# Kernel optimization log

Measured on AMD Instinct MI355X. Metric: run time of the kernel, lower is better.

## Reference

```python
import jax, jax.numpy as jnp
import numpy as np

N_HEADS = 16
D_EMBED = 1024
D_CROSS = 768
D_HEAD = D_EMBED // N_HEADS
B, S = 4, 2048


def setup_inputs() -> dict:
    key = jax.random.key(0)
    ks = jax.random.split(key, 10)
    sq = lambda k, shp, fan: jax.random.normal(k, shp, jnp.float32) / np.sqrt(fan)
    return {
        "x": jax.random.normal(ks[0], (B, S, D_EMBED), jnp.float32),
        "y": jax.random.normal(ks[1], (B, S, D_CROSS), jnp.float32),
        "Wq": sq(ks[2], (D_EMBED, D_EMBED), D_EMBED),
        "bq": jnp.zeros((D_EMBED,), jnp.float32),
        "Wk": sq(ks[3], (D_CROSS, D_EMBED), D_CROSS),
        "bk": jnp.zeros((D_EMBED,), jnp.float32),
        "Wv": sq(ks[4], (D_CROSS, D_EMBED), D_CROSS),
        "bv": jnp.zeros((D_EMBED,), jnp.float32),
        "Wo": sq(ks[5], (D_EMBED, D_EMBED), D_EMBED),
        "bo": jnp.zeros((D_EMBED,), jnp.float32),
    }


def reference(x, y, Wq, bq, Wk, bk, Wv, bv, Wo, bo):
    b, s, _ = y.shape
    q = x @ Wq + bq  # [b, s, d_embed]
    k = y @ Wk + bk
    v = y @ Wv + bv
    # [b, h, s, d_head]
    q = q.reshape(b, s, N_HEADS, D_HEAD).transpose(0, 2, 1, 3)
    k = k.reshape(b, s, N_HEADS, D_HEAD).transpose(0, 2, 1, 3)
    v = v.reshape(b, s, N_HEADS, D_HEAD).transpose(0, 2, 1, 3)
    scale = 1.0 / np.sqrt(D_HEAD).astype(np.float32)
    scores = jnp.einsum("bhqd,bhkd->bhqk", q, k) * scale
    weights = jax.nn.softmax(scores, axis=-1)
    out = jnp.einsum("bhqk,bhkd->bhqd", weights, v)
    out = out.transpose(0, 2, 1, 3).reshape(x.shape)
    return out @ Wo + bo
```

## Files before the change

### kernel.cpp

```cpp
#include <hip/hip_runtime.h>

#define NHEADS 16
#define DEMBED 1024
#define DCROSS 768
#define DHEAD  64
#define BATCH  4
#define SLEN   2048
#define MROWS  (BATCH * SLEN)

using bf16   = __bf16;
using bf16x8 = __attribute__((ext_vector_type(8))) __bf16;
using bf16x4 = __attribute__((ext_vector_type(4))) __bf16;
using bf16x2 = __attribute__((ext_vector_type(2))) __bf16;
using f32x4  = __attribute__((ext_vector_type(4))) float;
using f32x16 = __attribute__((ext_vector_type(16))) float;

__device__ __forceinline__ f32x4 mfma_bf16(bf16x8 a, bf16x8 b, f32x4 c) {
    return __builtin_amdgcn_mfma_f32_16x16x32_bf16(a, b, c, 0, 0, 0);
}
__device__ __forceinline__ f32x16 mfma32(bf16x8 a, bf16x8 b, f32x16 c) {
    return __builtin_amdgcn_mfma_f32_32x32x16_bf16(a, b, c, 0, 0, 0);
}

__device__ __forceinline__ void gl2lds16(const void* g, void* l) {
    __builtin_amdgcn_global_load_lds(
        (const __attribute__((address_space(1))) void*)g,
        (__attribute__((address_space(3))) void*)l, 16, 0, 0);
}

struct PrepArgs {
    const float* wsrc[4]; bf16* wdst[4]; int wK[4];
    const float *x, *y; bf16 *xb, *yb;
};
#define NTRB 4096
__global__ void prep_all(PrepArgs a) {
    const int bid = blockIdx.x;
    const int tid = threadIdx.x;
    if (bid < NTRB) {
        __shared__ float tile[32][33];
        const int which = bid >> 10, rem = bid & 1023;
        const int K = a.wK[which], N = DEMBED;
        const int n0 = (rem & 31) * 32, k0 = (rem >> 5) * 32;
        if (k0 >= K) return;
        const float* W = a.wsrc[which];
        bf16* Wt = a.wdst[which];
        const int tx = tid & 31, ty = tid >> 5;
#pragma unroll
        for (int i = 0; i < 32; i += 8)
            tile[ty + i][tx] = W[(size_t)(k0 + ty + i) * N + n0 + tx];
        __syncthreads();
#pragma unroll
        for (int i = 0; i < 32; i += 8)
            Wt[(size_t)(n0 + ty + i) * K + k0 + tx] = (bf16)tile[tx][ty + i];
    } else {
        const int n4x = MROWS * DEMBED / 4;
        const int n4y = MROWS * DCROSS / 4;
        int i = (bid - NTRB) * 256 + tid;
        const float* src; bf16* dst; int j;
        if (i < n4x) { src = a.x; dst = a.xb; j = i; }
        else { j = i - n4x; if (j >= n4y) return; src = a.y; dst = a.yb; }
        float4 v = ((const float4*)src)[j];
        bf16x4 o = { (bf16)v.x, (bf16)v.y, (bf16)v.z, (bf16)v.w };
        ((bf16x4*)dst)[j] = o;
    }
}

struct QkvArgs {
    const bf16 *xb, *yb, *Wqt, *Wkt, *Wvt;
    const float *bq, *bk, *bv;
    bf16 *Qb, *Kb, *Vt;
    float qscale;
};
__global__ __launch_bounds__(256, 3) void gemm_qkv(QkvArgs a) {
    __shared__ bf16 As[128 * 64];
    __shared__ bf16 Bs[128 * 64];
    const int id = blockIdx.x;
    const int cls = id >> 9;
    const bf16 *A, *Bt;
    const float* bias;
    int K, m0, n0;
    if (cls == 0) { int t = id;        m0 = (t >> 3) * 128; n0 = (t & 7) * 128;
                    A = a.xb;  Bt = a.Wqt; bias = a.bq; K = DEMBED; }
    else if (cls == 1) { int t = id - 512;  m0 = (t >> 3) * 128; n0 = (t & 7) * 128;
                    A = a.yb;  Bt = a.Wkt; bias = a.bk; K = DCROSS; }
    else { int t = id - 1024; m0 = (t >> 6) * 128; n0 = (t & 63) * 128;
                    A = a.Wvt; Bt = a.yb;  bias = a.bv; K = DCROSS; }

    const int tid  = threadIdx.x;
    const int wave = tid >> 6, lane = tid & 63;
    const int quad = lane >> 4, l15 = lane & 15;
    const int wr = wave >> 1, wc = wave & 1;

    const int srow = wave * 8 + (lane >> 3);
    const int scol = ((lane & 7) ^ (lane >> 3)) * 8;
    char* ldsA0 = (char*)As + wave * 1024;
    char* ldsB0 = (char*)Bs + wave * 1024;
    const bf16* gA0 = A + (size_t)(m0 + srow) * K + scol;
    const bf16* gB0 = Bt + (size_t)(n0 + srow) * K + scol;

    const int sw = l15 & 7;

    f32x4 acc[4][4] = {};

    for (int kt = 0; kt < K; kt += 64) {
        __syncthreads();
#pragma unroll
        for (int c = 0; c < 4; c++)
            gl2lds16(gA0 + (size_t)c * 32 * K + kt, ldsA0 + c * 4096);
#pragma unroll
        for (int c = 0; c < 4; c++)
            gl2lds16(gB0 + (size_t)c * 32 * K + kt, ldsB0 + c * 4096);
        __syncthreads();

#pragma unroll
        for (int kg = 0; kg < 2; kg++) {
            bf16x8 af[4], bfr[4];
#pragma unroll
            for (int i = 0; i < 4; i++)
                af[i] = *(const bf16x8*)((const char*)As +
                         (wr * 64 + i * 16 + l15) * 128 + (((kg * 4 + quad) ^ sw) * 16));
#pragma unroll
            for (int i = 0; i < 4; i++)
                bfr[i] = *(const bf16x8*)((const char*)Bs +
                         (wc * 64 + i * 16 + l15) * 128 + (((kg * 4 + quad) ^ sw) * 16));
#pragma unroll
            for (int fr = 0; fr < 4; fr++)
#pragma unroll
                for (int fc = 0; fc < 4; fc++)
                    acc[fr][fc] = mfma_bf16(af[fr], bfr[fc], acc[fr][fc]);
        }
    }

    if (cls < 2) {
        bf16* Cout = (cls == 0) ? a.Qb : a.Kb;
        const float alpha = (cls == 0) ? a.qscale : 1.0f;
#pragma unroll
        for (int fr = 0; fr < 4; fr++) {
            int row = m0 + wr * 64 + fr * 16 + quad * 4;
#pragma unroll
            for (int fc = 0; fc < 4; fc++) {
                int col = n0 + wc * 64 + fc * 16 + l15;
                float bv = bias[col];
#pragma unroll
                for (int r = 0; r < 4; r++)
                    Cout[(size_t)(row + r) * DEMBED + col] =
                        (bf16)((acc[fr][fc][r] + bv) * alpha);
            }
        }
    } else {
        const int b = n0 >> 11;
        const size_t bbase = (size_t)b * DEMBED * SLEN;
#pragma unroll
        for (int fr = 0; fr < 4; fr++) {
            int row = m0 + wr * 64 + fr * 16 + quad * 4;
#pragma unroll
            for (int fc = 0; fc < 4; fc++) {
                int col = n0 + wc * 64 + fc * 16 + l15;
                int s = col & (SLEN - 1);
#pragma unroll
                for (int r = 0; r < 4; r++)
                    a.Vt[bbase + (size_t)(row + r) * SLEN + s] =
                        (bf16)(acc[fr][fc][r] + bias[row + r]);
            }
        }
    }
}

__global__ __launch_bounds__(256, 3) void gemm_o(const bf16* __restrict__ A,
                                                 const bf16* __restrict__ Bt,
                                                 const float* __restrict__ bias,
                                                 float* __restrict__ Cout) {
    const int K = DEMBED, N = DEMBED;
    __shared__ bf16 As[128 * 64];
    __shared__ bf16 Bs[128 * 64];
    const int tid  = threadIdx.x;
    const int wave = tid >> 6, lane = tid & 63;
    const int quad = lane >> 4, l15 = lane & 15;
    const int m0 = blockIdx.x * 128, n0 = blockIdx.y * 128;
    const int wr = wave >> 1, wc = wave & 1;

    const int srow = wave * 8 + (lane >> 3);
    const int scol = ((lane & 7) ^ (lane >> 3)) * 8;
    char* ldsA0 = (char*)As + wave * 1024;
    char* ldsB0 = (char*)Bs + wave * 1024;
    const bf16* gA0 = A + (size_t)(m0 + srow) * K + scol;
    const bf16* gB0 = Bt + (size_t)(n0 + srow) * K + scol;

    const int sw = l15 & 7;

    f32x4 acc[4][4] = {};

    for (int kt = 0; kt < K; kt += 64) {
        __syncthreads();
#pragma unroll
        for (int c = 0; c < 4; c++)
            gl2lds16(gA0 + (size_t)c * 32 * K + kt, ldsA0 + c * 4096);
#pragma unroll
        for (int c = 0; c < 4; c++)
            gl2lds16(gB0 + (size_t)c * 32 * K + kt, ldsB0 + c * 4096);
        __syncthreads();

#pragma unroll
        for (int kg = 0; kg < 2; kg++) {
            bf16x8 af[4], bfr[4];
#pragma unroll
            for (int i = 0; i < 4; i++)
                af[i] = *(const bf16x8*)((const char*)As +
                         (wr * 64 + i * 16 + l15) * 128 + (((kg * 4 + quad) ^ sw) * 16));
#pragma unroll
            for (int i = 0; i < 4; i++)
                bfr[i] = *(const bf16x8*)((const char*)Bs +
                         (wc * 64 + i * 16 + l15) * 128 + (((kg * 4 + quad) ^ sw) * 16));
#pragma unroll
            for (int fr = 0; fr < 4; fr++)
#pragma unroll
                for (int fc = 0; fc < 4; fc++)
                    acc[fr][fc] = mfma_bf16(af[fr], bfr[fc], acc[fr][fc]);
        }
    }

#pragma unroll
    for (int fr = 0; fr < 4; fr++) {
        int row = m0 + wr * 64 + fr * 16 + quad * 4;
#pragma unroll
        for (int fc = 0; fc < 4; fc++) {
            int col = n0 + wc * 64 + fc * 16 + l15;
            float bv = bias[col];
#pragma unroll
            for (int r = 0; r < 4; r++)
                Cout[(size_t)(row + r) * N + col] = acc[fr][fc][r] + bv;
        }
    }
}

__global__ __launch_bounds__(128, 2) void attn(const bf16* __restrict__ Q,
                                               const bf16* __restrict__ K,
                                               const bf16* __restrict__ Vt,
                                               bf16* __restrict__ O) {
    __shared__ bf16 KsA[2][64 * 64];
    __shared__ bf16 VsA[2][64 * 64];

    const int tid  = threadIdx.x;
    const int wave = tid >> 6, lane = tid & 63;
    const int l31  = lane & 31, H = lane >> 5;
    const int bh = blockIdx.x, b = bh >> 4, h = bh & 15;
    const size_t rowbase = (size_t)b * SLEN;
    const int qb = blockIdx.y * 128 + wave * 64;
    const int hc = h * DHEAD;

    bf16x8 qf[2][4];
#pragma unroll
    for (int qs = 0; qs < 2; qs++)
#pragma unroll
        for (int ks = 0; ks < 4; ks++)
            qf[qs][ks] = *(const bf16x8*)(Q + (rowbase + qb + qs * 32 + l31) * DEMBED
                                          + hc + ks * 16 + H * 8);

    f32x16 o00 = {}, o01 = {}, o10 = {}, o11 = {};
    float lsv0 = 0.0f, lsv1 = 0.0f;

    const bf16* Kbase = K + rowbase * DEMBED + hc;
    const bf16* Vbase = Vt + (size_t)bh * DHEAD * SLEN;

    const int grow = tid >> 3;
    const int xcol = ((tid & 7) ^ (grow & 7)) * 8;
    const bf16* gK = Kbase + (size_t)grow * DEMBED + xcol;
    const bf16* gV = Vbase + (size_t)grow * SLEN + xcol;

    const int swz = l31 & 7;

    auto STAGE = [&](int buf, int kb) {
        char* lk = (char*)KsA + buf * 8192 + wave * 1024;
        char* lv = (char*)VsA + buf * 8192 + wave * 1024;
#pragma unroll
        for (int c = 0; c < 4; c++) {
            gl2lds16(gK + (size_t)(kb + c * 16) * DEMBED, lk + c * 2048);
            gl2lds16(gV + (size_t)(c * 16) * SLEN + kb,   lv + c * 2048);
        }
    };

    auto expPack = [&](const f32x16& s, int* c, float& l) {
#pragma unroll
        for (int t = 0; t < 8; t++) {
            float e0 = __builtin_amdgcn_exp2f(s[2 * t]);
            float e1 = __builtin_amdgcn_exp2f(s[2 * t + 1]);
            l += e0 + e1;
            union { bf16x2 h; int i; } p;
            p.h[0] = (bf16)e0; p.h[1] = (bf16)e1;
            c[t] = p.i;
        }
    };

    auto pvpair = [&](const int* cc, int ksl, bf16x8 vf0, bf16x8 vf1,
                      f32x16& oo0, f32x16& oo1) {
        auto w0 = __builtin_amdgcn_permlane32_swap(cc[4 * ksl + 0],
                                                   cc[4 * ksl + 2], false, false);
        auto w1 = __builtin_amdgcn_permlane32_swap(cc[4 * ksl + 1],
                                                   cc[4 * ksl + 3], false, false);
        union { int i[4]; bf16x8 v; } ap;
        ap.i[0] = w0[0]; ap.i[1] = w1[0]; ap.i[2] = w0[1]; ap.i[3] = w1[1];
        __builtin_amdgcn_s_setprio(1);
        oo0 = mfma32(ap.v, vf0, oo0);
        oo1 = mfma32(ap.v, vf1, oo1);
        __builtin_amdgcn_s_setprio(0);
    };

    STAGE(0, 0);
    __syncthreads();

    int cur = 0;
    for (int kb = 0; kb < SLEN; kb += 64) {
        if (kb + 64 < SLEN) STAGE(cur ^ 1, kb + 64);

        const char* Kbuf = (const char*)KsA + cur * 8192;
        const char* Vbuf = (const char*)VsA + cur * 8192;

        f32x16 s00 = {}, s01 = {}, s10 = {}, s11 = {};
        __builtin_amdgcn_s_setprio(1);
#pragma unroll
        for (int ks = 0; ks < 4; ks++) {
            const int slot = ((2 * ks + H) ^ swz) * 16;
            bf16x8 kf0 = *(const bf16x8*)(Kbuf + l31 * 128 + slot);
            bf16x8 kf1 = *(const bf16x8*)(Kbuf + (32 + l31) * 128 + slot);
            s00 = mfma32(kf0, qf[0][ks], s00);
            s01 = mfma32(kf1, qf[0][ks], s01);
            s10 = mfma32(kf0, qf[1][ks], s10);
            s11 = mfma32(kf1, qf[1][ks], s11);
        }
        __builtin_amdgcn_s_setprio(0);

        int cA0[8], cA1[8], cB0[8], cB1[8];

        expPack(s00, cA0, lsv0);
        expPack(s10, cA1, lsv1);

#pragma unroll
        for (int ks = 0; ks < 4; ks++) {
            if (ks == 1) expPack(s01, cB0, lsv0);
            if (ks == 2) expPack(s11, cB1, lsv1);
            const int slot = ((2 * ks + H) ^ swz) * 16;
            bf16x8 vf0 = *(const bf16x8*)(Vbuf + l31 * 128 + slot);
            bf16x8 vf1 = *(const bf16x8*)(Vbuf + (32 + l31) * 128 + slot);
            const int* u0 = (ks < 2) ? cA0 : cB0;
            const int* u1 = (ks < 2) ? cA1 : cB1;
            const int ksl = ks & 1;
            pvpair(u0, ksl, vf0, vf1, o00, o01);
            pvpair(u1, ksl, vf0, vf1, o10, o11);
        }

        __syncthreads();
        cur ^= 1;
    }

    lsv0 += __shfl_xor(lsv0, 32);
    lsv1 += __shfl_xor(lsv1, 32);
    float inv0 = 1.0f / lsv0;
    float inv1 = 1.0f / lsv1;
#pragma unroll
    for (int r = 0; r < 16; r++) {
        const int ql = (r & 3) + 8 * (r >> 2) + 4 * H;
        float iv0 = __shfl(inv0, ql);
        float iv1 = __shfl(inv1, ql);
        O[(rowbase + qb + ql) * DEMBED + hc + l31]      = (bf16)(o00[r] * iv0);
        O[(rowbase + qb + ql) * DEMBED + hc + 32 + l31] = (bf16)(o01[r] * iv0);
        O[(rowbase + qb + 32 + ql) * DEMBED + hc + l31]      = (bf16)(o10[r] * iv1);
        O[(rowbase + qb + 32 + ql) * DEMBED + hc + 32 + l31] = (bf16)(o11[r] * iv1);
    }
}

extern "C" void kernel_launch(void* const* d_in, const int* in_sizes, int n_in,
                              void* d_out, int out_size, void* d_ws, size_t ws_size,
                              hipStream_t stream) {
    const float* x  = (const float*)d_in[0];
    const float* y  = (const float*)d_in[1];
    const float* Wq = (const float*)d_in[2];
    const float* bq = (const float*)d_in[3];
    const float* Wk = (const float*)d_in[4];
    const float* bk = (const float*)d_in[5];
    const float* Wv = (const float*)d_in[6];
    const float* bv = (const float*)d_in[7];
    const float* Wo = (const float*)d_in[8];
    const float* bo = (const float*)d_in[9];
    float* out = (float*)d_out;

    char* ws = (char*)d_ws;
    size_t off = 0;
    auto alloc = [&](size_t bytes) {
        void* p = ws + off;
        off += (bytes + 255) & ~(size_t)255;
        return p;
    };
    bf16* xb  = (bf16*)alloc((size_t)MROWS * DEMBED * 2);
    bf16* yb  = (bf16*)alloc((size_t)MROWS * DCROSS * 2);
    bf16* Wqt = (bf16*)alloc((size_t)DEMBED * DEMBED * 2);
    bf16* Wkt = (bf16*)alloc((size_t)DEMBED * DCROSS * 2);
    bf16* Wvt = (bf16*)alloc((size_t)DEMBED * DCROSS * 2);
    bf16* Wot = (bf16*)alloc((size_t)DEMBED * DEMBED * 2);
    bf16* Qb  = (bf16*)alloc((size_t)MROWS * DEMBED * 2);
    bf16* Kb  = (bf16*)alloc((size_t)MROWS * DEMBED * 2);
    bf16* Vtb = (bf16*)alloc((size_t)MROWS * DEMBED * 2);
    bf16* Ab  = (bf16*)alloc((size_t)MROWS * DEMBED * 2);
    if (off > ws_size) return;

    {
        PrepArgs a;
        a.wsrc[0] = Wq; a.wdst[0] = Wqt; a.wK[0] = DEMBED;
        a.wsrc[1] = Wk; a.wdst[1] = Wkt; a.wK[1] = DCROSS;
        a.wsrc[2] = Wv; a.wdst[2] = Wvt; a.wK[2] = DCROSS;
        a.wsrc[3] = Wo; a.wdst[3] = Wot; a.wK[3] = DEMBED;
        a.x = x; a.y = y; a.xb = xb; a.yb = yb;
        int ncvt = (MROWS * DEMBED / 4 + MROWS * DCROSS / 4 + 255) / 256;
        prep_all<<<NTRB + ncvt, 256, 0, stream>>>(a);
    }

    {
        QkvArgs a;
        a.xb = xb; a.yb = yb; a.Wqt = Wqt; a.Wkt = Wkt; a.Wvt = Wvt;
        a.bq = bq; a.bk = bk; a.bv = bv;
        a.Qb = Qb; a.Kb = Kb; a.Vt = Vtb;
        a.qscale = 0.125f * 1.4426950408889634f;
        gemm_qkv<<<1536, 256, 0, stream>>>(a);
    }

    attn<<<dim3(BATCH * NHEADS, SLEN / 128), 128, 0, stream>>>(Qb, Kb, Vtb, Ab);

    gemm_o<<<dim3(MROWS / 128, DEMBED / 128), 256, 0, stream>>>(Ab, Wot, bo, out);
}
```

Baseline: 281.8 us.

## Enlarge GEMM tiles to 256x256 and 256x128 with 512-thread blocks and block swizzle

The QKV projection GEMM now uses 256x256 output tiles computed by 8 waves. Each wave holds a 128x64 accumulator and loads A fragments one row-block at a time to limit register pressure. Block IDs are remapped so consecutive blocks spread across the three projection classes. The output projection GEMM moves to 256x128 tiles with 512 threads. The aim is more data reuse per LDS load and less global traffic, at the cost of higher register use, lower occupancy, and fewer blocks in flight (384 and 256).

Measured after the change: 301.5 us. +7.0%, slower.

```diff
diff --git a/kernel.cpp b/kernel.cpp
--- a/kernel.cpp
+++ b/kernel.cpp
@@ -71,63 +71,64 @@
     bf16 *Qb, *Kb, *Vt;
     float qscale;
 };
-__global__ __launch_bounds__(256, 3) void gemm_qkv(QkvArgs a) {
-    __shared__ bf16 As[128 * 64];
-    __shared__ bf16 Bs[128 * 64];
-    const int id = blockIdx.x;
-    const int cls = id >> 9;
+__global__ __launch_bounds__(512, 2) void gemm_qkv(QkvArgs a) {
+    __shared__ bf16 As[256 * 64];
+    __shared__ bf16 Bs[256 * 64];
+    const int rb = blockIdx.x;
+    const int bid = (rb & 7) * 48 + (rb >> 3);
+    const int cls = bid >> 7;
+    const int t = bid & 127;
     const bf16 *A, *Bt;
     const float* bias;
     int K, m0, n0;
-    if (cls == 0) { int t = id;        m0 = (t >> 3) * 128; n0 = (t & 7) * 128;
-                    A = a.xb;  Bt = a.Wqt; bias = a.bq; K = DEMBED; }
-    else if (cls == 1) { int t = id - 512;  m0 = (t >> 3) * 128; n0 = (t & 7) * 128;
-                    A = a.yb;  Bt = a.Wkt; bias = a.bk; K = DCROSS; }
-    else { int t = id - 1024; m0 = (t >> 6) * 128; n0 = (t & 63) * 128;
-                    A = a.Wvt; Bt = a.yb;  bias = a.bv; K = DCROSS; }
+    if (cls == 0)      { m0 = (t >> 2) << 8; n0 = (t & 3) << 8;
+                         A = a.xb;  Bt = a.Wqt; bias = a.bq; K = DEMBED; }
+    else if (cls == 1) { m0 = (t >> 2) << 8; n0 = (t & 3) << 8;
+                         A = a.yb;  Bt = a.Wkt; bias = a.bk; K = DCROSS; }
+    else               { m0 = (t >> 5) << 8; n0 = (t & 31) << 8;
+                         A = a.Wvt; Bt = a.yb;  bias = a.bv; K = DCROSS; }
 
     const int tid  = threadIdx.x;
     const int wave = tid >> 6, lane = tid & 63;
     const int quad = lane >> 4, l15 = lane & 15;
-    const int wr = wave >> 1, wc = wave & 1;
-
-    const int srow = wave * 8 + (lane >> 3);
-    const int scol = ((lane & 7) ^ (lane >> 3)) * 8;
+    const int wr = wave >> 2, wcn = wave & 3;
+
+    const int srow = tid >> 3;
+    const int gcol = ((tid & 7) ^ (srow & 7)) * 8;
     char* ldsA0 = (char*)As + wave * 1024;
     char* ldsB0 = (char*)Bs + wave * 1024;
-    const bf16* gA0 = A + (size_t)(m0 + srow) * K + scol;
-    const bf16* gB0 = Bt + (size_t)(n0 + srow) * K + scol;
+    const bf16* gA0 = A + (size_t)(m0 + srow) * K + gcol;
+    const bf16* gB0 = Bt + (size_t)(n0 + srow) * K + gcol;
 
     const int sw = l15 & 7;
 
-    f32x4 acc[4][4] = {};
+    f32x4 acc[8][4] = {};
 
     for (int kt = 0; kt < K; kt += 64) {
         __syncthreads();
 #pragma unroll
         for (int c = 0; c < 4; c++)
-            gl2lds16(gA0 + (size_t)c * 32 * K + kt, ldsA0 + c * 4096);
+            gl2lds16(gA0 + (size_t)c * 64 * K + kt, ldsA0 + c * 8192);
 #pragma unroll
         for (int c = 0; c < 4; c++)
-            gl2lds16(gB0 + (size_t)c * 32 * K + kt, ldsB0 + c * 4096);
+            gl2lds16(gB0 + (size_t)c * 64 * K + kt, ldsB0 + c * 8192);
         __syncthreads();
 
 #pragma unroll
         for (int kg = 0; kg < 2; kg++) {
-            bf16x8 af[4], bfr[4];
-#pragma unroll
-            for (int i = 0; i < 4; i++)
-                af[i] = *(const bf16x8*)((const char*)As +
-                         (wr * 64 + i * 16 + l15) * 128 + (((kg * 4 + quad) ^ sw) * 16));
+            bf16x8 bfr[4];
 #pragma unroll
             for (int i = 0; i < 4; i++)
                 bfr[i] = *(const bf16x8*)((const char*)Bs +
-                         (wc * 64 + i * 16 + l15) * 128 + (((kg * 4 + quad) ^ sw) * 16));
-#pragma unroll
-            for (int fr = 0; fr < 4; fr++)
+                         (wcn * 64 + i * 16 + l15) * 128 + (((kg * 4 + quad) ^ sw) * 16));
+#pragma unroll
+            for (int fr = 0; fr < 8; fr++) {
+                bf16x8 af = *(const bf16x8*)((const char*)As +
+                         (wr * 128 + fr * 16 + l15) * 128 + (((kg * 4 + quad) ^ sw) * 16));
 #pragma unroll
                 for (int fc = 0; fc < 4; fc++)
-                    acc[fr][fc] = mfma_bf16(af[fr], bfr[fc], acc[fr][fc]);
+                    acc[fr][fc] = mfma_bf16(af, bfr[fc], acc[fr][fc]);
+            }
         }
     }
 
@@ -135,11 +136,11 @@
         bf16* Cout = (cls == 0) ? a.Qb : a.Kb;
         const float alpha = (cls == 0) ? a.qscale : 1.0f;
 #pragma unroll
-        for (int fr = 0; fr < 4; fr++) {
-            int row = m0 + wr * 64 + fr * 16 + quad * 4;
+        for (int fr = 0; fr < 8; fr++) {
+            int row = m0 + wr * 128 + fr * 16 + quad * 4;
 #pragma unroll
             for (int fc = 0; fc < 4; fc++) {
-                int col = n0 + wc * 64 + fc * 16 + l15;
+                int col = n0 + wcn * 64 + fc * 16 + l15;
                 float bv = bias[col];
 #pragma unroll
                 for (int r = 0; r < 4; r++)
@@ -151,11 +152,11 @@
         const int b = n0 >> 11;
         const size_t bbase = (size_t)b * DEMBED * SLEN;
 #pragma unroll
-        for (int fr = 0; fr < 4; fr++) {
-            int row = m0 + wr * 64 + fr * 16 + quad * 4;
+        for (int fr = 0; fr < 8; fr++) {
+            int row = m0 + wr * 128 + fr * 16 + quad * 4;
 #pragma unroll
             for (int fc = 0; fc < 4; fc++) {
-                int col = n0 + wc * 64 + fc * 16 + l15;
+                int col = n0 + wcn * 64 + fc * 16 + l15;
                 int s = col & (SLEN - 1);
 #pragma unroll
                 for (int r = 0; r < 4; r++)
@@ -166,25 +167,25 @@
     }
 }
 
-__global__ __launch_bounds__(256, 3) void gemm_o(const bf16* __restrict__ A,
+__global__ __launch_bounds__(512, 2) void gemm_o(const bf16* __restrict__ A,
                                                  const bf16* __restrict__ Bt,
                                                  const float* __restrict__ bias,
                                                  float* __restrict__ Cout) {
     const int K = DEMBED, N = DEMBED;
-    __shared__ bf16 As[128 * 64];
+    __shared__ bf16 As[256 * 64];
     __shared__ bf16 Bs[128 * 64];
     const int tid  = threadIdx.x;
     const int wave = tid >> 6, lane = tid & 63;
     const int quad = lane >> 4, l15 = lane & 15;
-    const int m0 = blockIdx.x * 128, n0 = blockIdx.y * 128;
-    const int wr = wave >> 1, wc = wave & 1;
-
-    const int srow = wave * 8 + (lane >> 3);
-    const int scol = ((lane & 7) ^ (lane >> 3)) * 8;
+    const int m0 = blockIdx.x * 256, n0 = blockIdx.y * 128;
+    const int wr = wave >> 1, wcn = wave & 1;
+
+    const int srow = tid >> 3;
+    const int gcol = ((tid & 7) ^ (srow & 7)) * 8;
     char* ldsA0 = (char*)As + wave * 1024;
     char* ldsB0 = (char*)Bs + wave * 1024;
-    const bf16* gA0 = A + (size_t)(m0 + srow) * K + scol;
-    const bf16* gB0 = Bt + (size_t)(n0 + srow) * K + scol;
+    const bf16* gA0 = A + (size_t)(m0 + srow) * K + gcol;
+    const bf16* gB0 = Bt + (size_t)(n0 + srow) * K + gcol;
 
     const int sw = l15 & 7;
 
@@ -194,28 +195,27 @@
         __syncthreads();
 #pragma unroll
         for (int c = 0; c < 4; c++)
-            gl2lds16(gA0 + (size_t)c * 32 * K + kt, ldsA0 + c * 4096);
-#pragma unroll
-        for (int c = 0; c < 4; c++)
-            gl2lds16(gB0 + (size_t)c * 32 * K + kt, ldsB0 + c * 4096);
+            gl2lds16(gA0 + (size_t)c * 64 * K + kt, ldsA0 + c * 8192);
+#pragma unroll
+        for (int c = 0; c < 2; c++)
+            gl2lds16(gB0 + (size_t)c * 64 * K + kt, ldsB0 + c * 8192);
         __syncthreads();
 
 #pragma unroll
         for (int kg = 0; kg < 2; kg++) {
-            bf16x8 af[4], bfr[4];
-#pragma unroll
-            for (int i = 0; i < 4; i++)
-                af[i] = *(const bf16x8*)((const char*)As +
-                         (wr * 64 + i * 16 + l15) * 128 + (((kg * 4 + quad) ^ sw) * 16));
+            bf16x8 bfr[4];
 #pragma unroll
             for (int i = 0; i < 4; i++)
                 bfr[i] = *(const bf16x8*)((const char*)Bs +
-                         (wc * 64 + i * 16 + l15) * 128 + (((kg * 4 + quad) ^ sw) * 16));
-#pragma unroll
-            for (int fr = 0; fr < 4; fr++)
+                         (wcn * 64 + i * 16 + l15) * 128 + (((kg * 4 + quad) ^ sw) * 16));
+#pragma unroll
+            for (int fr = 0; fr < 4; fr++) {
+                bf16x8 af = *(const bf16x8*)((const char*)As +
+                         (wr * 64 + fr * 16 + l15) * 128 + (((kg * 4 + quad) ^ sw) * 16));
 #pragma unroll
                 for (int fc = 0; fc < 4; fc++)
-                    acc[fr][fc] = mfma_bf16(af[fr], bfr[fc], acc[fr][fc]);
+                    acc[fr][fc] = mfma_bf16(af, bfr[fc], acc[fr][fc]);
+            }
         }
     }
 
@@ -224,7 +224,7 @@
         int row = m0 + wr * 64 + fr * 16 + quad * 4;
 #pragma unroll
         for (int fc = 0; fc < 4; fc++) {
-            int col = n0 + wc * 64 + fc * 16 + l15;
+            int col = n0 + wcn * 64 + fc * 16 + l15;
             float bv = bias[col];
 #pragma unroll
             for (int r = 0; r < 4; r++)
@@ -419,10 +419,10 @@
         a.bq = bq; a.bk = bk; a.bv = bv;
         a.Qb = Qb; a.Kb = Kb; a.Vt = Vtb;
         a.qscale = 0.125f * 1.4426950408889634f;
-        gemm_qkv<<<1536, 256, 0, stream>>>(a);
+        gemm_qkv<<<384, 512, 0, stream>>>(a);
     }
 
     attn<<<dim3(BATCH * NHEADS, SLEN / 128), 128, 0, stream>>>(Qb, Kb, Vtb, Ab);
 
-    gemm_o<<<dim3(MROWS / 128, DEMBED / 128), 256, 0, stream>>>(Ab, Wot, bo, out);
-}
+    gemm_o<<<dim3(MROWS / 256, DEMBED / 128), 512, 0, stream>>>(Ab, Wot, bo, out);
+}
```
